# Optimization experiments

Measured on AMD Instinct MI355X. Metric: run time of the kernel, lower is better.

Reference implementation:

```python
import jax, jax.numpy as jnp
import numpy as np

TEMPERATURE = 0.1
LOSS_WEIGHT = 1.0


def setup_inputs() -> dict:
    key = jax.random.key(0)
    k1, k2 = jax.random.split(key)
    B, M, N, C = 8, 4096, 4096, 3
    pred_points = jax.random.normal(k1, (B, M, C), dtype=jnp.float32)
    gt_points = jax.random.normal(k2, (B, N, C), dtype=jnp.float32)
    return {"pred_points": pred_points, "gt_points": gt_points}


def _cdist(x, y):
    # Euclidean distance matrix [B, M, N] via the |x|^2 + |y|^2 - 2<x,y> identity
    x2 = jnp.sum(x * x, axis=-1)  # [B, M]
    y2 = jnp.sum(y * y, axis=-1)  # [B, N]
    xy = jnp.einsum('bmc,bnc->bmn', x, y)  # [B, M, N]
    d2 = x2[:, :, None] + y2[:, None, :] - 2.0 * xy
    return jnp.sqrt(jnp.maximum(d2, 0.0))


def reference(pred_points, gt_points):
    dists = _cdist(pred_points, gt_points)                # [B, M, N]
    soft_assign = jax.nn.softmax(-dists / TEMPERATURE, axis=2)  # softmin
    weighted = jnp.sum(soft_assign * dists, axis=2)       # [B, M]
    per_batch = jnp.mean(weighted, axis=1)                # [B]
    return jnp.mean(per_batch) * LOSS_WEIGHT              # scalar ('mean' reduction)
```

## Files before the change

### kernel.cpp

```cpp
#include <hip/hip_runtime.h>
#include <hip/hip_bf16.h>

#ifndef __has_builtin
#define __has_builtin(x) 0
#endif

#if __has_builtin(__builtin_amdgcn_exp2f)
#define FAST_EXP2(x) __builtin_amdgcn_exp2f(x)
#else
#define FAST_EXP2(x) exp2f(x)
#endif

#if __has_builtin(__builtin_amdgcn_sqrtf)
#define FAST_SQRT(x) __builtin_amdgcn_sqrtf(x)
#else
#define FAST_SQRT(x) sqrtf(x)
#endif

constexpr int kB = 8;
constexpr int kM = 4096;
constexpr int kN = 4096;
constexpr int ROWS    = 64;
constexpr int CHUNKS  = 16;
constexpr int BLOCKT  = ROWS * CHUNKS;
constexpr int NPC     = kN / CHUNKS;
constexpr int NBLOCKS = (kB * kM) / ROWS;
constexpr float C2  = 14.426950408889634f;
constexpr float C22 = C2 * C2;
#define POISON_U32 0xAAAAAAAAu

__global__ __launch_bounds__(BLOCKT, 8) void emd_softmin_kernel(
    const float* __restrict__ pred, const float* __restrict__ gt,
    float* __restrict__ ws, float* __restrict__ out) {
  __shared__ __align__(16) float4 g4[kN];
  __shared__ float red_l[CHUNKS][ROWS];
  __shared__ float red_a[CHUNKS][ROWS];

  const int tid   = threadIdx.x;
  const int lane  = tid & 63;
  const int chunk = tid >> 6;
  const int rbase = blockIdx.x * ROWS;
  const int b     = rbase >> 12;
  const int m     = (rbase & (kM - 1)) + lane;

  const float* gtb = gt + (size_t)b * kN * 3;
  for (int i = tid; i < kN; i += BLOCKT) {
    const float* p = gtb + 3 * i;
    float x = p[0], y = p[1], z = p[2];
    float q = C22 * fmaf(x, x, fmaf(y, y, z * z));
    g4[i] = make_float4(x, y, z, q);
  }
  const float* pp_ptr = pred + ((size_t)b * kM + (size_t)m) * 3;
  const float px = pp_ptr[0], py = pp_ptr[1], pz = pp_ptr[2];
  const float nx = -2.0f * C22 * px;
  const float ny = -2.0f * C22 * py;
  const float nz = -2.0f * C22 * pz;
  const float pp = C22 * fmaf(px, px, fmaf(py, py, pz * pz));
  __syncthreads();

  float l0 = 0.f, l1 = 0.f, l2 = 0.f, l3 = 0.f;
  float a0 = 0.f, a1 = 0.f, a2 = 0.f, a3 = 0.f;
  const int n0 = chunk * NPC;
#pragma unroll 2
  for (int n = n0; n < n0 + NPC; n += 4) {
    const float4 G0 = g4[n + 0];
    const float4 G1 = g4[n + 1];
    const float4 G2 = g4[n + 2];
    const float4 G3 = g4[n + 3];
#define BODY(G, L, A)                                                 \
    {                                                                 \
      float s  = fmaf(nx, G.x, fmaf(ny, G.y, fmaf(nz, G.z, G.w + pp))); \
      float ds = FAST_SQRT(fmaxf(s, 0.0f));             \
      float p  = FAST_EXP2(-ds);                     \
      L += p;                                                         \
      A = fmaf(ds, p, A);                                             \
    }
    BODY(G0, l0, a0) BODY(G1, l1, a1) BODY(G2, l2, a2) BODY(G3, l3, a3)
#undef BODY
  }

  red_l[chunk][lane] = (l0 + l1) + (l2 + l3);
  red_a[chunk][lane] = (a0 + a1) + (a2 + a3);
  __syncthreads();

  if (tid < ROWS) {
    float lt = 0.f, at = 0.f;
#pragma unroll
    for (int c = 0; c < CHUNKS; ++c) { lt += red_l[c][tid]; at += red_a[c][tid]; }
    float w = (at / lt) * (1.0f / (C2 * kB * kM));
#pragma unroll
    for (int off = 32; off > 0; off >>= 1) w += __shfl_down(w, off, 64);
    if (tid == 0) {
      atomicAdd(&ws[0], w);
      __threadfence();
      unsigned t = atomicAdd((unsigned int*)(ws + 1), 1u);
      if (t == POISON_U32 + (unsigned)(NBLOCKS - 1)) {
        __threadfence();
        float s = atomicAdd(&ws[0], 0.0f);
        out[0] = s;
      }
    }
  }
}

extern "C" void kernel_launch(void* const* d_in, const int* in_sizes, int n_in,
                              void* d_out, int out_size, void* d_ws, size_t ws_size,
                              hipStream_t stream) {
  const float* pred = (const float*)d_in[0];
  const float* gt   = (const float*)d_in[1];
  float* out = (float*)d_out;
  float* ws  = (float*)d_ws;
  emd_softmin_kernel<<<NBLOCKS, BLOCKT, 0, stream>>>(pred, gt, ws, out);
}
```

Before: 97.44 us.

## Register-block four rows per thread and split N across blocks with combine pass

Each thread now handles four pred rows at once, so every gt point read from LDS feeds four distance/exp evaluations instead of one. The N dimension is split in two across blocks, giving 256 blocks with a half-size LDS tile, and a second small kernel combines the partial sums and does the final reduction. This is meant to cut LDS load traffic per useful op and keep occupancy up. It costs an extra kernel launch, global round-trips for the partial sums, and more registers per thread. A single-kernel fallback is kept for when the workspace is too small.

```diff
diff --git a/kernel.cpp b/kernel.cpp
--- a/kernel.cpp
+++ b/kernel.cpp
@@ -20,84 +20,189 @@
 constexpr int kB = 8;
 constexpr int kM = 4096;
 constexpr int kN = 4096;
-constexpr int ROWS    = 64;
-constexpr int CHUNKS  = 16;
-constexpr int BLOCKT  = ROWS * CHUNKS;
-constexpr int NPC     = kN / CHUNKS;
-constexpr int NBLOCKS = (kB * kM) / ROWS;
 constexpr float C2  = 14.426950408889634f;
 constexpr float C22 = C2 * C2;
 #define POISON_U32 0xAAAAAAAAu
 
-__global__ __launch_bounds__(BLOCKT, 8) void emd_softmin_kernel(
+constexpr int RPL    = 4;
+constexpr int ROWS   = 64 * RPL;
+constexpr int WAVES  = 16;
+constexpr int BLOCKT = 64 * WAVES;
+constexpr int NSPLIT = 2;
+constexpr int SEGN   = kN / NSPLIT;
+constexpr int NPC    = SEGN / WAVES;
+constexpr int NROWG  = (kB * kM) / ROWS;
+constexpr int NBLOCKS = NROWG * NSPLIT;
+constexpr int    PART_OFF = 16;
+constexpr size_t WS_NEED  = (size_t)(PART_OFF + 2 * NSPLIT * kB * kM) * 4;
+
+__global__ __launch_bounds__(BLOCKT, 4) void emd_partial_kernel(
+    const float* __restrict__ pred, const float* __restrict__ gt,
+    float* __restrict__ partL, float* __restrict__ partA) {
+  __shared__ __align__(16) float4 g4[SEGN];
+  __shared__ float red_l[WAVES][64][RPL];
+  __shared__ float red_a[WAVES][64][RPL];
+
+  const int tid  = threadIdx.x;
+  const int lane = tid & 63;
+  const int wv   = tid >> 6;
+  const int rg   = blockIdx.x >> 1;
+  const int seg  = blockIdx.x & 1;
+  const int rbase = rg * ROWS;
+  const int b     = rbase >> 12;
+
+  const float* gtb = gt + ((size_t)b * kN + (size_t)seg * SEGN) * 3;
+  for (int i = tid; i < SEGN; i += BLOCKT) {
+    const float* p = gtb + 3 * i;
+    float x = p[0], y = p[1], z = p[2];
+    g4[i] = make_float4(x, y, z, C22 * fmaf(x, x, fmaf(y, y, z * z)));
+  }
+  float nx[RPL], ny[RPL], nz[RPL], pq[RPL];
+  const int m0 = (rbase & (kM - 1)) + lane;
+#pragma unroll
+  for (int r = 0; r < RPL; ++r) {
+    const float* pp = pred + ((size_t)b * kM + m0 + r * 64) * 3;
+    float x = pp[0], y = pp[1], z = pp[2];
+    nx[r] = -2.0f * C22 * x;
+    ny[r] = -2.0f * C22 * y;
+    nz[r] = -2.0f * C22 * z;
+    pq[r] = C22 * fmaf(x, x, fmaf(y, y, z * z));
+  }
+  __syncthreads();
+
+  float l[RPL] = {0.f, 0.f, 0.f, 0.f};
+  float a[RPL] = {0.f, 0.f, 0.f, 0.f};
+  const int n0 = wv * NPC;
+#pragma unroll 2
+  for (int n = n0; n < n0 + NPC; n += 2) {
+    const float4 G0 = g4[n];
+    const float4 G1 = g4[n + 1];
+#pragma unroll
+    for (int r = 0; r < RPL; ++r) {
+      {
+        float s  = fmaf(nx[r], G0.x, fmaf(ny[r], G0.y, fmaf(nz[r], G0.z, G0.w + pq[r])));
+        float ds = FAST_SQRT(fmaxf(s, 0.0f));
+        float p  = FAST_EXP2(-ds);
+        l[r] += p;
+        a[r] = fmaf(ds, p, a[r]);
+      }
+      {
+        float s  = fmaf(nx[r], G1.x, fmaf(ny[r], G1.y, fmaf(nz[r], G1.z, G1.w + pq[r])));
+        float ds = FAST_SQRT(fmaxf(s, 0.0f));
+        float p  = FAST_EXP2(-ds);
+        l[r] += p;
+        a[r] = fmaf(ds, p, a[r]);
+      }
+    }
+  }
+#pragma unroll
+  for (int r = 0; r < RPL; ++r) {
+    red_l[wv][lane][r] = l[r];
+    red_a[wv][lane][r] = a[r];
+  }
+  __syncthreads();
+
+  if (tid < 64 * RPL) {
+    const int ln = tid & 63, r = tid >> 6;
+    float lt = 0.f, at = 0.f;
+#pragma unroll
+    for (int c = 0; c < WAVES; ++c) { lt += red_l[c][ln][r]; at += red_a[c][ln][r]; }
+    const int row = rbase + r * 64 + ln;
+    partL[(size_t)seg * (kB * kM) + row] = lt;
+    partA[(size_t)seg * (kB * kM) + row] = at;
+  }
+}
+
+constexpr int CB      = 512;
+constexpr int CBLOCKS = (kB * kM) / CB;
+__global__ __launch_bounds__(CB) void emd_combine_kernel(
+    const float* __restrict__ partL, const float* __restrict__ partA,
+    float* __restrict__ ws, float* __restrict__ out) {
+  const int row = blockIdx.x * CB + threadIdx.x;
+  float lt = partL[row] + partL[kB * kM + row];
+  float at = partA[row] + partA[kB * kM + row];
+  float w = (at / lt) * (1.0f / (C2 * (float)(kB * kM)));
+#pragma unroll
+  for (int off = 32; off > 0; off >>= 1) w += __shfl_down(w, off, 64);
+  __shared__ float sred[CB / 64];
+  const int lane = threadIdx.x & 63, wv = threadIdx.x >> 6;
+  if (lane == 0) sred[wv] = w;
+  __syncthreads();
+  if (threadIdx.x == 0) {
+    float s = 0.f;
+#pragma unroll
+    for (int i = 0; i < CB / 64; ++i) s += sred[i];
+    atomicAdd(&ws[0], s);
+    __threadfence();
+    unsigned t = atomicAdd((unsigned int*)(ws + 1), 1u);
+    if (t == POISON_U32 + (unsigned)(CBLOCKS - 1)) {
+      __threadfence();
+      out[0] = atomicAdd(&ws[0], 0.0f);
+    }
+  }
+}
+
+constexpr int F_CHUNKS  = 16;
+constexpr int F_BLOCKT  = 64 * F_CHUNKS;
+constexpr int F_NPC     = kN / F_CHUNKS;
+constexpr int F_NBLOCKS = (kB * kM) / 64;
+
+__global__ __launch_bounds__(F_BLOCKT, 8) void emd_softmin_fallback(
     const float* __restrict__ pred, const float* __restrict__ gt,
     float* __restrict__ ws, float* __restrict__ out) {
   __shared__ __align__(16) float4 g4[kN];
-  __shared__ float red_l[CHUNKS][ROWS];
-  __shared__ float red_a[CHUNKS][ROWS];
-
-  const int tid   = threadIdx.x;
-  const int lane  = tid & 63;
-  const int chunk = tid >> 6;
-  const int rbase = blockIdx.x * ROWS;
-  const int b     = rbase >> 12;
-  const int m     = (rbase & (kM - 1)) + lane;
-
+  __shared__ float red_l[F_CHUNKS][64];
+  __shared__ float red_a[F_CHUNKS][64];
+  const int tid = threadIdx.x, lane = tid & 63, chunk = tid >> 6;
+  const int rbase = blockIdx.x * 64;
+  const int b = rbase >> 12;
+  const int m = (rbase & (kM - 1)) + lane;
   const float* gtb = gt + (size_t)b * kN * 3;
-  for (int i = tid; i < kN; i += BLOCKT) {
+  for (int i = tid; i < kN; i += F_BLOCKT) {
     const float* p = gtb + 3 * i;
     float x = p[0], y = p[1], z = p[2];
-    float q = C22 * fmaf(x, x, fmaf(y, y, z * z));
-    g4[i] = make_float4(x, y, z, q);
+    g4[i] = make_float4(x, y, z, C22 * fmaf(x, x, fmaf(y, y, z * z)));
   }
   const float* pp_ptr = pred + ((size_t)b * kM + (size_t)m) * 3;
   const float px = pp_ptr[0], py = pp_ptr[1], pz = pp_ptr[2];
-  const float nx = -2.0f * C22 * px;
-  const float ny = -2.0f * C22 * py;
-  const float nz = -2.0f * C22 * pz;
-  const float pp = C22 * fmaf(px, px, fmaf(py, py, pz * pz));
-  __syncthreads();
-
-  float l0 = 0.f, l1 = 0.f, l2 = 0.f, l3 = 0.f;
-  float a0 = 0.f, a1 = 0.f, a2 = 0.f, a3 = 0.f;
-  const int n0 = chunk * NPC;
+  const float nx = -2.0f * C22 * px, ny = -2.0f * C22 * py, nz = -2.0f * C22 * pz;
+  const float pq = C22 * fmaf(px, px, fmaf(py, py, pz * pz));
+  __syncthreads();
+  float l0 = 0.f, l1 = 0.f, a0 = 0.f, a1 = 0.f;
+  const int n0 = chunk * F_NPC;
 #pragma unroll 2
-  for (int n = n0; n < n0 + NPC; n += 4) {
-    const float4 G0 = g4[n + 0];
-    const float4 G1 = g4[n + 1];
-    const float4 G2 = g4[n + 2];
-    const float4 G3 = g4[n + 3];
-#define BODY(G, L, A)                                                 \
-    {                                                                 \
-      float s  = fmaf(nx, G.x, fmaf(ny, G.y, fmaf(nz, G.z, G.w + pp))); \
-      float ds = FAST_SQRT(fmaxf(s, 0.0f));             \
-      float p  = FAST_EXP2(-ds);                     \
-      L += p;                                                         \
-      A = fmaf(ds, p, A);                                             \
-    }
-    BODY(G0, l0, a0) BODY(G1, l1, a1) BODY(G2, l2, a2) BODY(G3, l3, a3)
-#undef BODY
-  }
-
-  red_l[chunk][lane] = (l0 + l1) + (l2 + l3);
-  red_a[chunk][lane] = (a0 + a1) + (a2 + a3);
-  __syncthreads();
-
-  if (tid < ROWS) {
+  for (int n = n0; n < n0 + F_NPC; n += 2) {
+    const float4 G0 = g4[n], G1 = g4[n + 1];
+    {
+      float s = fmaf(nx, G0.x, fmaf(ny, G0.y, fmaf(nz, G0.z, G0.w + pq)));
+      float ds = FAST_SQRT(fmaxf(s, 0.f));
+      float p = FAST_EXP2(-ds);
+      l0 += p; a0 = fmaf(ds, p, a0);
+    }
+    {
+      float s = fmaf(nx, G1.x, fmaf(ny, G1.y, fmaf(nz, G1.z, G1.w + pq)));
+      float ds = FAST_SQRT(fmaxf(s, 0.f));
+      float p = FAST_EXP2(-ds);
+      l1 += p; a1 = fmaf(ds, p, a1);
+    }
+  }
+  red_l[chunk][lane] = l0 + l1;
+  red_a[chunk][lane] = a0 + a1;
+  __syncthreads();
+  if (tid < 64) {
     float lt = 0.f, at = 0.f;
 #pragma unroll
-    for (int c = 0; c < CHUNKS; ++c) { lt += red_l[c][tid]; at += red_a[c][tid]; }
-    float w = (at / lt) * (1.0f / (C2 * kB * kM));
+    for (int c = 0; c < F_CHUNKS; ++c) { lt += red_l[c][tid]; at += red_a[c][tid]; }
+    float w = (at / lt) * (1.0f / (C2 * (float)(kB * kM)));
 #pragma unroll
     for (int off = 32; off > 0; off >>= 1) w += __shfl_down(w, off, 64);
     if (tid == 0) {
       atomicAdd(&ws[0], w);
       __threadfence();
       unsigned t = atomicAdd((unsigned int*)(ws + 1), 1u);
-      if (t == POISON_U32 + (unsigned)(NBLOCKS - 1)) {
+      if (t == POISON_U32 + (unsigned)(F_NBLOCKS - 1)) {
         __threadfence();
-        float s = atomicAdd(&ws[0], 0.0f);
-        out[0] = s;
+        out[0] = atomicAdd(&ws[0], 0.0f);
       }
     }
   }
@@ -110,5 +215,13 @@
   const float* gt   = (const float*)d_in[1];
   float* out = (float*)d_out;
   float* ws  = (float*)d_ws;
-  emd_softmin_kernel<<<NBLOCKS, BLOCKT, 0, stream>>>(pred, gt, ws, out);
-}
+
+  if (ws_size >= WS_NEED) {
+    float* partL = ws + PART_OFF;
+    float* partA = partL + (size_t)NSPLIT * kB * kM;
+    emd_partial_kernel<<<NBLOCKS, BLOCKT, 0, stream>>>(pred, gt, partL, partA);
+    emd_combine_kernel<<<CBLOCKS, CB, 0, stream>>>(partL, partA, ws, out);
+  } else {
+    emd_softmin_fallback<<<F_NBLOCKS, F_BLOCKT, 0, stream>>>(pred, gt, ws, out);
+  }
+}
```

After: 94.62 us. -2.9%, faster.
